# Kernel tuning notes

Measured on AMD Instinct MI355X. Metric: run time of the kernel, lower is better.

Reference implementation:

```python
import jax, jax.numpy as jnp
import numpy as np

L, B, E, H = 512, 32, 1024, 16
NEG = -1e9  # finite stand-in for masked_fill(-inf); avoids NaNs if a row were fully masked


def setup_inputs() -> dict:
    key = jax.random.key(0)
    ks = jax.random.split(key, 6)
    s_in = (2.0 / (3 * E + E)) ** 0.5   # xavier-ish scale for in_proj
    s_out = (2.0 / (E + E)) ** 0.5
    return {
        "query": jax.random.normal(ks[0], (L, B, E), jnp.float32),
        "key": jax.random.normal(ks[1], (L, B, E), jnp.float32),
        "value": jax.random.normal(ks[2], (L, B, E), jnp.float32),
        "attn_mask": jax.random.randint(ks[3], (B, L, L), 0, 2).astype(jnp.bool_),
        "in_proj_weight": jax.random.normal(ks[4], (3 * E, E), jnp.float32) * s_in,
        "in_proj_bias": jnp.zeros((3 * E,), jnp.float32),
        "out_proj_weight": jax.random.normal(ks[5], (E, E), jnp.float32) * s_out,
        "out_proj_bias": jnp.zeros((E,), jnp.float32),
        "num_heads": H,
    }


def reference(query, key, value, attn_mask, in_proj_weight, in_proj_bias,
              out_proj_weight, out_proj_bias, num_heads):
    Lq, Bz, Em = query.shape
    hd = Em // num_heads
    Wq, Wk, Wv = jnp.split(in_proj_weight, 3, axis=0)
    bq, bk, bv = jnp.split(in_proj_bias, 3, axis=0)
    # in-projection: x @ W^T + b  (torch F.linear convention)
    q = query @ Wq.T + bq
    k = key @ Wk.T + bk
    v = value @ Wv.T + bv
    # [L, B, E] -> [B*H, L, hd], batch-major (b*H + h) per torch view semantics
    def split_heads(x):
        return x.reshape(x.shape[0], Bz * num_heads, hd).transpose(1, 0, 2)
    q, k, v = split_heads(q), split_heads(k), split_heads(v)
    q = q / jnp.sqrt(jnp.asarray(hd, q.dtype))
    # scores: [B*H, Lq, Lk]
    attn = jnp.einsum('bqd,bkd->bqk', q, k)
    # mask broadcast to heads: [B, L, L] -> [B*H, L, L] with index b*H + h
    mask_mh = jnp.repeat(attn_mask, num_heads, axis=0)
    # original: scatter zeros where masked, then masked_fill(-inf) inside
    # multi_head_positional_attention; net effect = mask -> -inf before softmax
    attn = jnp.where(mask_mh, NEG, attn)
    p = jax.nn.softmax(attn, axis=-1)
    out = jnp.einsum('bqk,bkd->bqd', p, v)        # [B*H, Lq, hd]
    out = out.transpose(1, 0, 2).reshape(Lq, Bz, Em)
    out = out @ out_proj_weight.T + out_proj_bias  # [L, B, E]
    return out
```

## Files before the change

### kernel.cpp

```cpp
#include <hip/hip_runtime.h>
#include <hip/hip_bf16.h>
#include <stdint.h>

#define LSEQ 512
#define BATCH 32
#define EMB 1024
#define NHEAD 16
#define HDIM 64
#define TOK (LSEQ*BATCH)
#define BHTOT (BATCH*NHEAD)

typedef __attribute__((ext_vector_type(8))) short short8;
typedef __attribute__((ext_vector_type(4))) short short4v;
typedef __attribute__((ext_vector_type(4))) float f32x4;

__device__ __forceinline__ short f2bf(float f) {
  __hip_bfloat16 h = __float2bfloat16(f);
  union { __hip_bfloat16 h; short s; } u; u.h = h;
  return u.s;
}

__device__ __forceinline__ short8 cvt8(f32x4 x0, f32x4 x1) {
  short8 o;
  o[0] = f2bf(x0[0]); o[1] = f2bf(x0[1]); o[2] = f2bf(x0[2]); o[3] = f2bf(x0[3]);
  o[4] = f2bf(x1[0]); o[5] = f2bf(x1[1]); o[6] = f2bf(x1[2]); o[7] = f2bf(x1[3]);
  return o;
}

#if defined(__has_builtin)
#if __has_builtin(__builtin_amdgcn_global_load_lds)
#define HAVE_GLL 1
#endif
#endif

__device__ __forceinline__ void gload_lds16(const void* g, void* l) {
#ifdef HAVE_GLL
  __builtin_amdgcn_global_load_lds((const __attribute__((address_space(1))) void*)g,
                                   (__attribute__((address_space(3))) void*)l, 16, 0, 0);
#else
  *(short8*)l = *(const short8*)g;
#endif
}

#define WAIT_VM8  do { asm volatile("s_waitcnt vmcnt(8)" ::: "memory"); __builtin_amdgcn_sched_barrier(0); } while (0)
#define WAIT_VM4  do { asm volatile("s_waitcnt vmcnt(4)" ::: "memory"); __builtin_amdgcn_sched_barrier(0); } while (0)
#define WAIT_VM0  do { asm volatile("s_waitcnt vmcnt(0)" ::: "memory"); __builtin_amdgcn_sched_barrier(0); } while (0)
#define WAIT_LGKM0 do { asm volatile("s_waitcnt lgkmcnt(0)" ::: "memory"); __builtin_amdgcn_sched_barrier(0); } while (0)
#define BAR() __builtin_amdgcn_s_barrier()

__global__ __launch_bounds__(256) void castx_kernel(const float* __restrict__ xq,
                                                    const float* __restrict__ xk,
                                                    const float* __restrict__ xv,
                                                    short* __restrict__ xb)
{
  const size_t i = blockIdx.x * 256 + threadIdx.x;
  #pragma unroll
  for (int it = 0; it < 6; ++it) {
    const float* src = (it < 2) ? xq : (it < 4) ? xk : xv;
    size_t p = i + (size_t)it * 1048576;
    size_t local = p - (size_t)(it >> 1) * 2097152;
    f32x4 x0 = ((const f32x4*)src)[2 * local];
    f32x4 x1 = ((const f32x4*)src)[2 * local + 1];
    ((short8*)xb)[p] = cvt8(x0, x1);
  }
}

__global__ __launch_bounds__(256) void prep2_kernel(const float* __restrict__ W,
                                                    const float* __restrict__ Wo,
                                                    const float* __restrict__ bias,
                                                    short* __restrict__ Wb, short* __restrict__ Wob,
                                                    float* __restrict__ biasp,
                                                    const int* __restrict__ mask,
                                                    uint32_t* __restrict__ mb)
{
  const int i = blockIdx.x * 256 + threadIdx.x;
  if (i < 786432) {
    f32x4 v = ((const f32x4*)W)[i];
    int row = i >> 8;
    float s = (row < 1024) ? 0.125f : 1.0f;
    short4v o;
    o[0] = f2bf(v[0]*s); o[1] = f2bf(v[1]*s); o[2] = f2bf(v[2]*s); o[3] = f2bf(v[3]*s);
    ((short4v*)Wb)[i] = o;
  } else {
    int j = i - 786432;
    f32x4 v = ((const f32x4*)Wo)[j];
    short4v o;
    o[0] = f2bf(v[0]); o[1] = f2bf(v[1]); o[2] = f2bf(v[2]); o[3] = f2bf(v[3]);
    ((short4v*)Wob)[j] = o;
  }
  if (i < 768) {
    f32x4 v = ((const f32x4*)bias)[i];
    float s = (i < 256) ? 0.125f : 1.0f;
    f32x4 o = {v[0]*s, v[1]*s, v[2]*s, v[3]*s};
    ((f32x4*)biasp)[i] = o;
  }
  {
    int w = i >> 6;
    int lane = threadIdx.x & 63;
    const int* src = mask + ((size_t)w << 9);
    uint32_t* dst = mb + w * 16;
    #pragma unroll
    for (int c = 0; c < 8; ++c) {
      int v = src[c * 64 + lane];
      unsigned long long m = __ballot(v != 0);
      if (lane == 0) dst[c*2]     = (uint32_t)m;
      if (lane == 1) dst[c*2 + 1] = (uint32_t)(m >> 32);
    }
  }
}


#define FRAG_READ(AsX, BsX)                                           \
    short8 af[4], bfr[4];                                             \
    _Pragma("unroll")                                                 \
    for (int mi = 0; mi < 4; ++mi) {                                  \
      int row = wm + mi * 16 + l15;                                   \
      int cs = l4 ^ ((row >> 1) & 3);                                 \
      af[mi] = *(const short8*)&AsX[row * 32 + cs * 8];               \
    }                                                                 \
    _Pragma("unroll")                                                 \
    for (int ni = 0; ni < 4; ++ni) {                                  \
      int row = wn + ni * 16 + l15;                                   \
      int cs = l4 ^ ((row >> 1) & 3);                                 \
      bfr[ni] = *(const short8*)&BsX[row * 32 + cs * 8];              \
    }

#define DO_MFMA()                                                     \
    _Pragma("unroll")                                                 \
    for (int mi = 0; mi < 4; ++mi)                                    \
      _Pragma("unroll")                                               \
      for (int ni = 0; ni < 4; ++ni)                                  \
        acc[mi][ni] = __builtin_amdgcn_mfma_f32_16x16x32_bf16(af[mi], bfr[ni], acc[mi][ni], 0, 0, 0)

#define ISSUE(AsX, BsX, koff)                                         \
    _Pragma("unroll")                                                 \
    for (int jj = 0; jj < 2; ++jj) {                                  \
      gload_lds16(aSrc[jj] + (koff), &AsX[sDst[jj]]);                 \
      gload_lds16(bSrc[jj] + (koff), &BsX[sDst[jj]]);                 \
    }

#define GSTEP_I(AsX, BsX, WAITM, koff)                                \
  { WAITM; BAR();                                                     \
    FRAG_READ(AsX, BsX);                                              \
    WAIT_LGKM0; BAR();                                                \
    ISSUE(AsX, BsX, koff);                                            \
    DO_MFMA(); }

#define GSTEP_N(AsX, BsX, WAITM)                                      \
  { WAITM; BAR();                                                     \
    FRAG_READ(AsX, BsX);                                              \
    WAIT_LGKM0; BAR();                                                \
    DO_MFMA(); }

#define STAGE_COORDS(Abase, Bbase)                                    \
  const short* aSrc[2]; const short* bSrc[2]; int sDst[2];            \
  _Pragma("unroll")                                                   \
  for (int jj = 0; jj < 2; ++jj) {                                    \
    int ch = tid + jj * 256;                                          \
    int row = ch >> 2, cl = ch & 3;                                   \
    int cs = cl ^ ((row >> 1) & 3);                                   \
    aSrc[jj] = (Abase) + (size_t)(m0 + row) * 1024 + cs * 8;          \
    bSrc[jj] = (Bbase) + (size_t)(n0 + row) * 1024 + cs * 8;          \
    sDst[jj] = ch * 8;                                                \
  }

#define PIPE_BODY()                                                   \
  ISSUE(As0, Bs0, 0); ISSUE(As1, Bs1, 32); ISSUE(As2, Bs2, 64);       \
  for (int i = 0; i < 9; ++i) {                                       \
    const int s = 3 * i;                                              \
    GSTEP_I(As0, Bs0, WAIT_VM8, (s + 3) * 32);                        \
    GSTEP_I(As1, Bs1, WAIT_VM8, (s + 4) * 32);                        \
    GSTEP_I(As2, Bs2, WAIT_VM8, (s + 5) * 32);                        \
  }                                                                   \
  GSTEP_I(As0, Bs0, WAIT_VM8, 30 * 32);                               \
  GSTEP_I(As1, Bs1, WAIT_VM8, 31 * 32);                               \
  GSTEP_N(As2, Bs2, WAIT_VM8);                                        \
  GSTEP_N(As0, Bs0, WAIT_VM4);                                        \
  GSTEP_N(As1, Bs1, WAIT_VM0);

__launch_bounds__(256, 3)
__global__ void proj_gemm(const short* __restrict__ A, const short* __restrict__ B,
                          const float* __restrict__ bp, short* __restrict__ C)
{
  int flat = blockIdx.y * 8 + blockIdx.x;
  int X = flat & 7, s0 = flat >> 3;
  int m0 = (X * 16 + (s0 >> 3)) * 128;
  int n0 = (s0 & 7) * 128;

  __shared__ alignas(16) short As0[128 * 32];
  __shared__ alignas(16) short As1[128 * 32];
  __shared__ alignas(16) short As2[128 * 32];
  __shared__ alignas(16) short Bs0[128 * 32];
  __shared__ alignas(16) short Bs1[128 * 32];
  __shared__ alignas(16) short Bs2[128 * 32];

  const int tid = threadIdx.x, lane = tid & 63;
  const int w = tid >> 6;
  const int wm = (w >> 1) * 64, wn = (w & 1) * 64;
  const int l15 = lane & 15, l4 = lane >> 4;

  STAGE_COORDS(A, B);

  f32x4 acc[4][4];
  #pragma unroll
  for (int mi = 0; mi < 4; ++mi)
    #pragma unroll
    for (int ni = 0; ni < 4; ++ni) acc[mi][ni] = f32x4{0.f, 0.f, 0.f, 0.f};

  PIPE_BODY();

  #pragma unroll
  for (int ni = 0; ni < 4; ++ni) {
    int gcol = n0 + wn + ni * 16 + l15;
    float bv = bp[gcol];
    int h = gcol >> 6, d = gcol & 63;
    #pragma unroll
    for (int mi = 0; mi < 4; ++mi) {
      int growb = m0 + wm + mi * 16 + l4 * 4;
      #pragma unroll
      for (int r = 0; r < 4; ++r) {
        int grow = growb + r;
        int lsq = grow >> 5, bb = grow & 31;
        C[((size_t)((bb * NHEAD + h) * LSEQ + lsq)) * HDIM + d] = f2bf(acc[mi][ni][r] + bv);
      }
    }
  }
}

__launch_bounds__(256, 3)
__global__ void out_gemm(const short* __restrict__ Ab, const short* __restrict__ W,
                         const float* __restrict__ bo, float* __restrict__ out)
{
  int flat = blockIdx.y * 8 + blockIdx.x;
  int X = flat & 7, s0 = flat >> 3;
  int m0 = (X * 16 + (s0 >> 3)) * 128;
  int n0 = (s0 & 7) * 128;

  __shared__ alignas(16) short As0[128 * 32];
  __shared__ alignas(16) short As1[128 * 32];
  __shared__ alignas(16) short As2[128 * 32];
  __shared__ alignas(16) short Bs0[128 * 32];
  __shared__ alignas(16) short Bs1[128 * 32];
  __shared__ alignas(16) short Bs2[128 * 32];

  const int tid = threadIdx.x, lane = tid & 63;
  const int w = tid >> 6;
  const int wm = (w >> 1) * 64, wn = (w & 1) * 64;
  const int l15 = lane & 15, l4 = lane >> 4;

  STAGE_COORDS(Ab, W);

  f32x4 acc[4][4];
  #pragma unroll
  for (int mi = 0; mi < 4; ++mi)
    #pragma unroll
    for (int ni = 0; ni < 4; ++ni) acc[mi][ni] = f32x4{0.f, 0.f, 0.f, 0.f};

  PIPE_BODY();

  #pragma unroll
  for (int ni = 0; ni < 4; ++ni) {
    int gcol = n0 + wn + ni * 16 + l15;
    float bv = bo[gcol];
    #pragma unroll
    for (int mi = 0; mi < 4; ++mi) {
      int growb = m0 + wm + mi * 16 + l4 * 4;
      #pragma unroll
      for (int r = 0; r < 4; ++r)
        out[(size_t)(growb + r) * 1024 + gcol] = acc[mi][ni][r] + bv;
    }
  }
}

__launch_bounds__(256, 2)
__global__ void attn_kernel(const short* __restrict__ qh, const short* __restrict__ kh,
                            const short* __restrict__ vh, const uint32_t* __restrict__ mb,
                            short* __restrict__ ao)
{
  int flat = blockIdx.y * 8 + blockIdx.x;
  int X = flat & 7, s = flat >> 3;
  int bh = X * 64 + (s >> 2);
  int qblk = s & 3;
  int b = bh >> 4, h = bh & 15;
  int q0 = qblk * 128;

  const int tid = threadIdx.x, lane = tid & 63, w = tid >> 6;
  const int l15 = lane & 15, l4 = lane >> 4;

  __shared__ alignas(16) short Ks[64 * 64];
  __shared__ alignas(16) short Vt[64 * 72];
  __shared__ alignas(16) short Ps[4 * 32 * 72];
  __shared__ uint32_t Mw[128 * 2];

  const size_t bhoff = (size_t)bh * (LSEQ * HDIM);

  short8 aq[2][2];
  #pragma unroll
  for (int m = 0; m < 2; ++m) {
    int qrow = q0 + w * 32 + m * 16 + l15;
    const short* qp = qh + bhoff + (size_t)qrow * HDIM + l4 * 8;
    aq[m][0] = *(const short8*)qp;
    aq[m][1] = *(const short8*)(qp + 32);
  }

  f32x4 oacc[2][4];
  float l_part[2][4];
  #pragma unroll
  for (int m = 0; m < 2; ++m) {
    #pragma unroll
    for (int n = 0; n < 4; ++n) oacc[m][n] = f32x4{0.f, 0.f, 0.f, 0.f};
    #pragma unroll
    for (int r = 0; r < 4; ++r) l_part[m][r] = 0.f;
  }

  for (int kt = 0; kt < 8; ++kt) {
    __syncthreads();
    #pragma unroll
    for (int jj = 0; jj < 2; ++jj) {
      int ch = tid + jj * 256;
      int row = ch >> 3, cl = ch & 7;
      int cg = cl ^ (row & 7);
      const short* g = kh + bhoff + (size_t)(kt * 64 + row) * HDIM + cg * 8;
      gload_lds16(g, &Ks[ch * 8]);
    }
    #pragma unroll
    for (int jj = 0; jj < 2; ++jj) {
      int c = tid + jj * 256;
      int kv = c & 63, d0 = (c >> 6) * 8;
      const short* g = vh + bhoff + (size_t)(kt * 64 + kv) * HDIM + d0;
      short8 vv = *(const short8*)g;
      #pragma unroll
      for (int j = 0; j < 8; ++j) Vt[(d0 + j) * 72 + kv] = vv[j];
    }
    {
      int qr = tid >> 1, wd = tid & 1;
      Mw[qr * 2 + wd] = mb[((size_t)b * LSEQ + q0 + qr) * 16 + kt * 2 + wd];
    }
    __syncthreads();

    f32x4 sa[2][4];
    #pragma unroll
    for (int m = 0; m < 2; ++m)
      #pragma unroll
      for (int n = 0; n < 4; ++n) sa[m][n] = f32x4{0.f, 0.f, 0.f, 0.f};
    #pragma unroll
    for (int ss = 0; ss < 2; ++ss) {
      #pragma unroll
      for (int n = 0; n < 4; ++n) {
        int row = n * 16 + l15;
        int cs = (ss * 4 + l4) ^ (row & 7);
        short8 bk = *(const short8*)&Ks[row * 64 + cs * 8];
        #pragma unroll
        for (int m = 0; m < 2; ++m)
          sa[m][n] = __builtin_amdgcn_mfma_f32_16x16x32_bf16(aq[m][ss], bk, sa[m][n], 0, 0, 0);
      }
    }

    #pragma unroll
    for (int m = 0; m < 2; ++m) {
      #pragma unroll
      for (int r = 0; r < 4; ++r) {
        int qr = w * 32 + m * 16 + l4 * 4 + r;
        uint32_t w0 = Mw[qr * 2] >> l15;
        uint32_t w1 = Mw[qr * 2 + 1] >> l15;
        float p0 = (w0 & 1u)        ? 0.f : __expf(sa[m][0][r]);
        float p1 = ((w0 >> 16) & 1u) ? 0.f : __expf(sa[m][1][r]);
        float p2 = (w1 & 1u)        ? 0.f : __expf(sa[m][2][r]);
        float p3 = ((w1 >> 16) & 1u) ? 0.f : __expf(sa[m][3][r]);
        l_part[m][r] += (p0 + p1) + (p2 + p3);
        short* pp = &Ps[w * 2304 + (m * 16 + l4 * 4 + r) * 72];
        pp[0 * 16 + l15] = f2bf(p0);
        pp[1 * 16 + l15] = f2bf(p1);
        pp[2 * 16 + l15] = f2bf(p2);
        pp[3 * 16 + l15] = f2bf(p3);
      }
    }

    #pragma unroll
    for (int ss = 0; ss < 2; ++ss) {
      short8 pa[2];
      #pragma unroll
      for (int m = 0; m < 2; ++m)
        pa[m] = *(const short8*)&Ps[w * 2304 + (m * 16 + l15) * 72 + ss * 32 + l4 * 8];
      #pragma unroll
      for (int n = 0; n < 4; ++n) {
        short8 bv = *(const short8*)&Vt[(n * 16 + l15) * 72 + ss * 32 + l4 * 8];
        #pragma unroll
        for (int m = 0; m < 2; ++m)
          oacc[m][n] = __builtin_amdgcn_mfma_f32_16x16x32_bf16(pa[m], bv, oacc[m][n], 0, 0, 0);
      }
    }
  }

  #pragma unroll
  for (int m = 0; m < 2; ++m) {
    #pragma unroll
    for (int r = 0; r < 4; ++r) {
      float l = l_part[m][r];
      #pragma unroll
      for (int off = 1; off < 16; off <<= 1) l += __shfl_xor(l, off, 64);
      float inv = 1.0f / fmaxf(l, 1e-30f);
      int qrow = q0 + w * 32 + m * 16 + l4 * 4 + r;
      size_t tbase = ((size_t)qrow * BATCH + b) * EMB + h * HDIM;
      #pragma unroll
      for (int n = 0; n < 4; ++n)
        ao[tbase + n * 16 + l15] = f2bf(oacc[m][n][r] * inv);
    }
  }
}

extern "C" void kernel_launch(void* const* d_in, const int* in_sizes, int n_in,
                              void* d_out, int out_size, void* d_ws, size_t ws_size,
                              hipStream_t stream) {
  const float* q_in = (const float*)d_in[0];
  const float* k_in = (const float*)d_in[1];
  const float* v_in = (const float*)d_in[2];
  const int*   mask = (const int*)d_in[3];
  const float* Wp   = (const float*)d_in[4];
  const float* bp   = (const float*)d_in[5];
  const float* Wo   = (const float*)d_in[6];
  const float* bo   = (const float*)d_in[7];

  char* ws = (char*)d_ws;
  short* Wb    = (short*)ws;    ws += (size_t)3072 * 1024 * 2;
  short* Wob   = (short*)ws;    ws += (size_t)1024 * 1024 * 2;
  float* biasp = (float*)ws;    ws += (size_t)3072 * 4;
  uint32_t* mb = (uint32_t*)ws; ws += (size_t)BATCH * LSEQ * 16 * 4;
  short* qh    = (short*)ws;    ws += (size_t)TOK * EMB * 2;
  short* kh    = (short*)ws;    ws += (size_t)TOK * EMB * 2;
  short* vh    = (short*)ws;    ws += (size_t)TOK * EMB * 2;
  short* xb    = (short*)ws;    ws += (size_t)3 * TOK * EMB * 2;
  short* ao    = xb;

  castx_kernel<<<4096, 256, 0, stream>>>(q_in, k_in, v_in, xb);
  prep2_kernel<<<4096, 256, 0, stream>>>(Wp, Wo, bp, Wb, Wob, biasp, mask, mb);
  proj_gemm<<<dim3(8, 128), 256, 0, stream>>>(xb,                       Wb,                biasp,        qh);
  proj_gemm<<<dim3(8, 128), 256, 0, stream>>>(xb + (size_t)TOK * EMB,   Wb + 1024 * 1024,  biasp + 1024, kh);
  proj_gemm<<<dim3(8, 128), 256, 0, stream>>>(xb + (size_t)2*TOK * EMB, Wb + 2*1024*1024,  biasp + 2048, vh);
  attn_kernel<<<dim3(8, 256), 256, 0, stream>>>(qh, kh, vh, mb, ao);
  out_gemm<<<dim3(8, 128), 256, 0, stream>>>(ao, Wob, bo, (float*)d_out);
}
```

Before: 326.3 us.

## Fuse fp32-to-bf16 activation cast into projection GEMM staging

Removes the separate castx kernel and has proj_gemm load fp32 activations straight into LDS, converting to bf16 when reading fragments. This drops one full write and re-read of the converted activations. In exchange, the A tile in LDS doubles in size, so the pipeline goes from three stages to two, and every k-step repeats the conversion. Separately, the attention kernel's launch-bounds occupancy hint is raised from 2 to 4 blocks per CU.

New measurement: 340.0 us. 4.2% more time.

```diff
diff --git a/kernel.cpp b/kernel.cpp
--- a/kernel.cpp
+++ b/kernel.cpp
@@ -43,27 +43,11 @@
 }
 
 #define WAIT_VM8  do { asm volatile("s_waitcnt vmcnt(8)" ::: "memory"); __builtin_amdgcn_sched_barrier(0); } while (0)
+#define WAIT_VM6  do { asm volatile("s_waitcnt vmcnt(6)" ::: "memory"); __builtin_amdgcn_sched_barrier(0); } while (0)
 #define WAIT_VM4  do { asm volatile("s_waitcnt vmcnt(4)" ::: "memory"); __builtin_amdgcn_sched_barrier(0); } while (0)
 #define WAIT_VM0  do { asm volatile("s_waitcnt vmcnt(0)" ::: "memory"); __builtin_amdgcn_sched_barrier(0); } while (0)
 #define WAIT_LGKM0 do { asm volatile("s_waitcnt lgkmcnt(0)" ::: "memory"); __builtin_amdgcn_sched_barrier(0); } while (0)
 #define BAR() __builtin_amdgcn_s_barrier()
-
-__global__ __launch_bounds__(256) void castx_kernel(const float* __restrict__ xq,
-                                                    const float* __restrict__ xk,
-                                                    const float* __restrict__ xv,
-                                                    short* __restrict__ xb)
-{
-  const size_t i = blockIdx.x * 256 + threadIdx.x;
-  #pragma unroll
-  for (int it = 0; it < 6; ++it) {
-    const float* src = (it < 2) ? xq : (it < 4) ? xk : xv;
-    size_t p = i + (size_t)it * 1048576;
-    size_t local = p - (size_t)(it >> 1) * 2097152;
-    f32x4 x0 = ((const f32x4*)src)[2 * local];
-    f32x4 x1 = ((const f32x4*)src)[2 * local + 1];
-    ((short8*)xb)[p] = cvt8(x0, x1);
-  }
-}
 
 __global__ __launch_bounds__(256) void prep2_kernel(const float* __restrict__ W,
                                                     const float* __restrict__ Wo,
@@ -164,22 +148,48 @@
     sDst[jj] = ch * 8;                                                \
   }
 
-#define PIPE_BODY()                                                   \
-  ISSUE(As0, Bs0, 0); ISSUE(As1, Bs1, 32); ISSUE(As2, Bs2, 64);       \
-  for (int i = 0; i < 9; ++i) {                                       \
-    const int s = 3 * i;                                              \
-    GSTEP_I(As0, Bs0, WAIT_VM8, (s + 3) * 32);                        \
-    GSTEP_I(As1, Bs1, WAIT_VM8, (s + 4) * 32);                        \
-    GSTEP_I(As2, Bs2, WAIT_VM8, (s + 5) * 32);                        \
-  }                                                                   \
-  GSTEP_I(As0, Bs0, WAIT_VM8, 30 * 32);                               \
-  GSTEP_I(As1, Bs1, WAIT_VM8, 31 * 32);                               \
-  GSTEP_N(As2, Bs2, WAIT_VM8);                                        \
-  GSTEP_N(As0, Bs0, WAIT_VM4);                                        \
-  GSTEP_N(As1, Bs1, WAIT_VM0);
+
+#define P_FRAG_READ(AsX, BsX)                                         \
+    short8 af[4], bfr[4];                                             \
+    _Pragma("unroll")                                                 \
+    for (int mi = 0; mi < 4; ++mi) {                                  \
+      int row = wm + mi * 16 + l15;                                   \
+      int r7 = row & 7;                                               \
+      int c0 = (l4 * 2) ^ r7, c1 = (l4 * 2 + 1) ^ r7;                 \
+      f32x4 x0 = *(const f32x4*)&AsX[row * 32 + c0 * 4];              \
+      f32x4 x1 = *(const f32x4*)&AsX[row * 32 + c1 * 4];              \
+      af[mi] = cvt8(x0, x1);                                          \
+    }                                                                 \
+    _Pragma("unroll")                                                 \
+    for (int ni = 0; ni < 4; ++ni) {                                  \
+      int row = wn + ni * 16 + l15;                                   \
+      int cs = l4 ^ ((row >> 1) & 3);                                 \
+      bfr[ni] = *(const short8*)&BsX[row * 32 + cs * 8];              \
+    }
+
+#define P_ISSUE(AsX, BsX, koff)                                       \
+    _Pragma("unroll")                                                 \
+    for (int jj = 0; jj < 4; ++jj)                                    \
+      gload_lds16(aSrc[jj] + (koff), &AsX[aDst[jj]]);                 \
+    _Pragma("unroll")                                                 \
+    for (int jj = 0; jj < 2; ++jj)                                    \
+      gload_lds16(bSrc[jj] + (koff), &BsX[bDst[jj]]);
+
+#define P_GSTEP_I(AsX, BsX, koff)                                     \
+  { WAIT_VM6; BAR();                                                  \
+    P_FRAG_READ(AsX, BsX);                                            \
+    WAIT_LGKM0; BAR();                                                \
+    P_ISSUE(AsX, BsX, koff);                                          \
+    DO_MFMA(); }
+
+#define P_GSTEP_N(AsX, BsX, WAITM)                                    \
+  { WAITM; BAR();                                                     \
+    P_FRAG_READ(AsX, BsX);                                            \
+    WAIT_LGKM0; BAR();                                                \
+    DO_MFMA(); }
 
 __launch_bounds__(256, 3)
-__global__ void proj_gemm(const short* __restrict__ A, const short* __restrict__ B,
+__global__ void proj_gemm(const float* __restrict__ A, const short* __restrict__ B,
                           const float* __restrict__ bp, short* __restrict__ C)
 {
   int flat = blockIdx.y * 8 + blockIdx.x;
@@ -187,19 +197,34 @@
   int m0 = (X * 16 + (s0 >> 3)) * 128;
   int n0 = (s0 & 7) * 128;
 
-  __shared__ alignas(16) short As0[128 * 32];
-  __shared__ alignas(16) short As1[128 * 32];
-  __shared__ alignas(16) short As2[128 * 32];
+  __shared__ alignas(16) float As0[128 * 32];
+  __shared__ alignas(16) float As1[128 * 32];
   __shared__ alignas(16) short Bs0[128 * 32];
   __shared__ alignas(16) short Bs1[128 * 32];
-  __shared__ alignas(16) short Bs2[128 * 32];
 
   const int tid = threadIdx.x, lane = tid & 63;
   const int w = tid >> 6;
   const int wm = (w >> 1) * 64, wn = (w & 1) * 64;
   const int l15 = lane & 15, l4 = lane >> 4;
 
-  STAGE_COORDS(A, B);
+  const float* aSrc[4]; int aDst[4];
+  #pragma unroll
+  for (int jj = 0; jj < 4; ++jj) {
+    int ch = tid + jj * 256;
+    int row = ch >> 3, cl = ch & 7;
+    int cs = cl ^ (row & 7);
+    aSrc[jj] = A + (size_t)(m0 + row) * 1024 + cs * 4;
+    aDst[jj] = ch * 4;
+  }
+  const short* bSrc[2]; int bDst[2];
+  #pragma unroll
+  for (int jj = 0; jj < 2; ++jj) {
+    int ch = tid + jj * 256;
+    int row = ch >> 2, cl = ch & 3;
+    int cs = cl ^ ((row >> 1) & 3);
+    bSrc[jj] = B + (size_t)(n0 + row) * 1024 + cs * 8;
+    bDst[jj] = ch * 8;
+  }
 
   f32x4 acc[4][4];
   #pragma unroll
@@ -207,7 +232,14 @@
     #pragma unroll
     for (int ni = 0; ni < 4; ++ni) acc[mi][ni] = f32x4{0.f, 0.f, 0.f, 0.f};
 
-  PIPE_BODY();
+  P_ISSUE(As0, Bs0, 0);
+  P_ISSUE(As1, Bs1, 32);
+  for (int i = 0; i < 15; ++i) {
+    P_GSTEP_I(As0, Bs0, (2 * i + 2) * 32);
+    P_GSTEP_I(As1, Bs1, (2 * i + 3) * 32);
+  }
+  P_GSTEP_N(As0, Bs0, WAIT_VM6);
+  P_GSTEP_N(As1, Bs1, WAIT_VM0);
 
   #pragma unroll
   for (int ni = 0; ni < 4; ++ni) {
@@ -256,7 +288,18 @@
     #pragma unroll
     for (int ni = 0; ni < 4; ++ni) acc[mi][ni] = f32x4{0.f, 0.f, 0.f, 0.f};
 
-  PIPE_BODY();
+  ISSUE(As0, Bs0, 0); ISSUE(As1, Bs1, 32); ISSUE(As2, Bs2, 64);
+  for (int i = 0; i < 9; ++i) {
+    const int s = 3 * i;
+    GSTEP_I(As0, Bs0, WAIT_VM8, (s + 3) * 32);
+    GSTEP_I(As1, Bs1, WAIT_VM8, (s + 4) * 32);
+    GSTEP_I(As2, Bs2, WAIT_VM8, (s + 5) * 32);
+  }
+  GSTEP_I(As0, Bs0, WAIT_VM8, 30 * 32);
+  GSTEP_I(As1, Bs1, WAIT_VM8, 31 * 32);
+  GSTEP_N(As2, Bs2, WAIT_VM8);
+  GSTEP_N(As0, Bs0, WAIT_VM4);
+  GSTEP_N(As1, Bs1, WAIT_VM0);
 
   #pragma unroll
   for (int ni = 0; ni < 4; ++ni) {
@@ -272,7 +315,7 @@
   }
 }
 
-__launch_bounds__(256, 2)
+__launch_bounds__(256, 4)
 __global__ void attn_kernel(const short* __restrict__ qh, const short* __restrict__ kh,
                             const short* __restrict__ vh, const uint32_t* __restrict__ mb,
                             short* __restrict__ ao)
@@ -429,14 +472,12 @@
   short* qh    = (short*)ws;    ws += (size_t)TOK * EMB * 2;
   short* kh    = (short*)ws;    ws += (size_t)TOK * EMB * 2;
   short* vh    = (short*)ws;    ws += (size_t)TOK * EMB * 2;
-  short* xb    = (short*)ws;    ws += (size_t)3 * TOK * EMB * 2;
-  short* ao    = xb;
-
-  castx_kernel<<<4096, 256, 0, stream>>>(q_in, k_in, v_in, xb);
+  short* ao    = (short*)ws;    ws += (size_t)TOK * EMB * 2;
+
   prep2_kernel<<<4096, 256, 0, stream>>>(Wp, Wo, bp, Wb, Wob, biasp, mask, mb);
-  proj_gemm<<<dim3(8, 128), 256, 0, stream>>>(xb,                       Wb,                biasp,        qh);
-  proj_gemm<<<dim3(8, 128), 256, 0, stream>>>(xb + (size_t)TOK * EMB,   Wb + 1024 * 1024,  biasp + 1024, kh);
-  proj_gemm<<<dim3(8, 128), 256, 0, stream>>>(xb + (size_t)2*TOK * EMB, Wb + 2*1024*1024,  biasp + 2048, vh);
+  proj_gemm<<<dim3(8, 128), 256, 0, stream>>>(q_in, Wb,                biasp,        qh);
+  proj_gemm<<<dim3(8, 128), 256, 0, stream>>>(k_in, Wb + 1024 * 1024,  biasp + 1024, kh);
+  proj_gemm<<<dim3(8, 128), 256, 0, stream>>>(v_in, Wb + 2*1024*1024,  biasp + 2048, vh);
   attn_kernel<<<dim3(8, 256), 256, 0, stream>>>(qh, kh, vh, mb, ao);
   out_gemm<<<dim3(8, 128), 256, 0, stream>>>(ao, Wob, bo, (float*)d_out);
 }
```
